# Performance work log

Hardware: AMD Instinct MI355X
Metric: run time of the kernel (lower is better)

## Reference

```python
import jax, jax.numpy as jnp
import numpy as np

N = 50000      # nodes (single node type 'tx')
E = 400000     # edges per edge type ('fwd' and 'rev')
F_IN = 128     # input feature dim
F = 128        # cfg.gnn.dim_inner
H = 8          # attention heads
D = F // H     # per-head dim
L = 2          # cfg.gnn.layers_mp
C = 2          # dim_out (fraud logits)


def setup_inputs() -> dict:
    key = jax.random.key(0)
    k = jax.random.split(key, 12)
    f32 = jnp.float32
    g = lambda kk, sh, fan: jax.random.normal(kk, sh, f32) / np.float32(np.sqrt(fan))
    return dict(
        x=jax.random.normal(k[0], (N, F_IN), f32),
        edge_index_fwd=jax.random.randint(k[1], (2, E), 0, N),
        edge_index_rev=jax.random.randint(k[2], (2, E), 0, N),
        in_w=g(k[3], (F_IN, F), F_IN),
        in_b=jnp.zeros((F,), f32),
        kqv_w=g(k[4], (L, F, 3 * F), F),
        kqv_b=jnp.zeros((L, 3 * F), f32),
        krel_w=g(k[5], (L, 2, H, D, D), D),
        vrel_w=g(k[6], (L, 2, H, D, D), D),
        p_rel=jnp.ones((L, 2, H), f32),
        out_w=g(k[7], (L, F, F), F),
        out_b=jnp.zeros((L, F), f32),
        skip=jnp.ones((L,), f32),
        head_w=g(k[8], (F, C), F),
        head_b=jnp.zeros((C,), f32),
    )


def reference(x, edge_index_fwd, edge_index_rev, in_w, in_b, kqv_w, kqv_b,
              krel_w, vrel_w, p_rel, out_w, out_b, skip, head_w, head_b):
    n = x.shape[0]
    ef, er = edge_index_fwd, edge_index_rev
    Ef, Er = ef.shape[1], er.shape[1]
    dst = jnp.concatenate([ef[1], er[1]])                 # [E_tot]
    scale = 1.0 / jnp.sqrt(jnp.asarray(D, x.dtype))

    h = x @ in_w + in_b                                   # in_proj['tx'], [N,F]
    for l in range(L):
        kqv = h @ kqv_w[l] + kqv_b[l]                     # [N,3F]
        k, q, v = jnp.split(kqv, 3, axis=1)
        k = k.reshape(n, H, D)
        q = q.reshape(n, H, D)
        v = v.reshape(n, H, D)
        # per-edge-type relation transforms (head-wise DxD, no bias)
        k_rel = jnp.einsum('nhd,ehdf->enhf', k, krel_w[l])  # [2,N,H,D]
        v_rel = jnp.einsum('nhd,ehdf->enhf', v, vrel_w[l])
        # gather src features per edge type, concatenate edge types
        k_j = jnp.concatenate([k_rel[0][ef[0]], k_rel[1][er[0]]], axis=0)  # [E_tot,H,D]
        v_j = jnp.concatenate([v_rel[0][ef[0]], v_rel[1][er[0]]], axis=0)
        p_e = jnp.concatenate([jnp.broadcast_to(p_rel[l, 0], (Ef, H)),
                               jnp.broadcast_to(p_rel[l, 1], (Er, H))], axis=0)
        q_i = q[dst]                                       # [E_tot,H,D]
        alpha = jnp.einsum('ehd,ehd->eh', q_i, k_j) * p_e * scale
        # segment softmax over all incoming edges of each dst node
        m = jax.ops.segment_max(alpha, dst, num_segments=n)
        ex = jnp.exp(alpha - m[dst])
        denom = jax.ops.segment_sum(ex, dst, num_segments=n)
        w = ex / (denom[dst] + 1e-16)                      # [E_tot,H]
        agg = jax.ops.segment_sum(w[:, :, None] * v_j, dst,
                                  num_segments=n).reshape(n, F)
        a = jax.nn.gelu(agg, approximate=False) @ out_w[l] + out_b[l]
        g = jax.nn.sigmoid(skip[l])
        h = jax.nn.relu(g * a + (1.0 - g) * h)             # skip + act(dropout=0)
    return h @ head_w + head_b                             # logits [N,C]
```

## Files before the change

kernel.cpp:

```cpp
#include <hip/hip_runtime.h>
#include <math.h>

typedef short short8 __attribute__((ext_vector_type(8)));
typedef float f32x4 __attribute__((ext_vector_type(4)));

__device__ __forceinline__ unsigned short f2bf(float f){
    unsigned u = __float_as_uint(f);
    unsigned r = u + 0x7fffu + ((u >> 16) & 1u);
    return (unsigned short)(r >> 16);
}

__global__ void k_count(const int* __restrict__ ef, const int* __restrict__ er,
                        int* __restrict__ deg, int Ef, int Er)
{
    int Etot = Ef + Er;
    for (int e = blockIdx.x*blockDim.x + threadIdx.x; e < Etot; e += gridDim.x*blockDim.x) {
        int dst = (e < Ef) ? ef[Ef + e] : er[Er + (e - Ef)];
        atomicAdd(&deg[dst], 1);
    }
}

__global__ void k_chunk_sums(const int* __restrict__ deg, int* __restrict__ csum, int n)
{
    __shared__ int s[256];
    int t = threadIdx.x, i = blockIdx.x*256 + t;
    s[t] = (i < n) ? deg[i] : 0;
    __syncthreads();
    for (int off = 128; off > 0; off >>= 1) {
        if (t < off) s[t] += s[t + off];
        __syncthreads();
    }
    if (t == 0) csum[blockIdx.x] = s[0];
}

__global__ void k_scan_chunks(int* __restrict__ csum, int nch)
{
    __shared__ int s[1024];
    int t = threadIdx.x;
    int v = (t < nch) ? csum[t] : 0;
    s[t] = v; __syncthreads();
    for (int off = 1; off < 1024; off <<= 1) {
        int u = (t >= off) ? s[t - off] : 0;
        __syncthreads();
        s[t] += u;
        __syncthreads();
    }
    if (t < nch) csum[t] = s[t] - v;
}

__global__ void k_rowstart(const int* __restrict__ deg, const int* __restrict__ csum,
                           int* __restrict__ row_start, int* __restrict__ cursor, int n)
{
    __shared__ int s[256];
    int t = threadIdx.x, i = blockIdx.x*256 + t;
    int d = (i < n) ? deg[i] : 0;
    s[t] = d; __syncthreads();
    for (int off = 1; off < 256; off <<= 1) {
        int u = (t >= off) ? s[t - off] : 0;
        __syncthreads();
        s[t] += u;
        __syncthreads();
    }
    if (i <= n) {
        int rs = csum[blockIdx.x] + s[t] - d;
        row_start[i] = rs;
        cursor[i] = rs;
    }
}

__global__ void k_fill(const int* __restrict__ ef, const int* __restrict__ er,
                       int* __restrict__ cursor, unsigned* __restrict__ srcs,
                       int Ef, int Er, int n_nodes)
{
    int Etot = Ef + Er;
    if (blockIdx.x == 0 && threadIdx.x == 0) { srcs[Etot] = 0; srcs[Etot + 1] = 0; }
    for (int e = blockIdx.x*blockDim.x + threadIdx.x; e < Etot; e += gridDim.x*blockDim.x) {
        int src, dst, tt;
        if (e < Ef) { src = ef[e]; dst = ef[Ef + e]; tt = 0; }
        else { int e2 = e - Ef; src = er[e2]; dst = er[Er + e2]; tt = 1; }
        int pos = atomicAdd(&cursor[dst], 1);
        srcs[pos] = (unsigned)(tt*n_nodes + src)*32u;
    }
}

__global__ void k_setup(const float* __restrict__ kqv_w, const float* __restrict__ kqv_b,
                        const float* __restrict__ krel_w, const float* __restrict__ vrel_w,
                        const float* __restrict__ p_rel, const float* __restrict__ out_w,
                        const float* __restrict__ out_b, const float* __restrict__ in_w,
                        const float* __restrict__ x, const float* __restrict__ head_b,
                        unsigned short* __restrict__ WcT, float* __restrict__ biasc,
                        unsigned short* __restrict__ WoT, float* __restrict__ biaso,
                        unsigned short* __restrict__ WiT, unsigned short* __restrict__ x16,
                        int* __restrict__ deg, float* __restrict__ logits, int n_nodes)
{
    const int N0 = 2*129*640;
    const int N1 = N0 + 2*129*128;
    const int N2 = N1 + 128*128;
    const long long N3 = (long long)N2 + (long long)n_nodes*32;
    const long long N4 = N3 + n_nodes;
    const long long N5 = N4 + 2*n_nodes;

    for (long long idx = (long long)blockIdx.x*blockDim.x + threadIdx.x; idx < N5;
         idx += (long long)gridDim.x*blockDim.x) {
        if (idx < N0) {
            int i = (int)idx;
            int l = i / (129*640);
            int rem = i % (129*640);
            int r = rem / 640, c = rem % 640;
            float val;
            if (c < 128) {
                val = (r < 128) ? kqv_w[((size_t)l*128 + r)*384 + 128 + c]
                                : kqv_b[l*384 + 128 + c];
            } else {
                int c2 = c - 128;
                int tt = c2 >> 8;
                int cc = c2 & 255;
                int f = cc >> 1;
                int part = cc & 1;
                int hh = f >> 4, fd = f & 15;
                const float* rw = (part == 0 ? krel_w : vrel_w)
                                  + (((size_t)(l*2 + tt)*8 + hh)*16)*16 + fd;
                int base_col = (part == 0 ? 0 : 256) + hh*16;
                float s = 0.f;
                #pragma unroll
                for (int d = 0; d < 16; ++d) {
                    float a = (r < 128) ? kqv_w[((size_t)l*128 + r)*384 + base_col + d]
                                        : kqv_b[l*384 + base_col + d];
                    s += a * rw[d*16];
                }
                if (part == 0) s *= p_rel[(l*2 + tt)*8 + hh] * 0.25f * 1.4426950408889634f;
                val = s;
            }
            if (r < 128) WcT[((size_t)l*640 + c)*128 + r] = f2bf(val);
            else         biasc[l*640 + c] = val;
        } else if (idx < N1) {
            int i = (int)(idx - N0);
            int l = i / (129*128);
            int rem = i % (129*128);
            int r = rem / 128, c = rem % 128;
            if (r < 128) WoT[((size_t)l*128 + c)*128 + r] = f2bf(out_w[((size_t)l*128 + r)*128 + c]);
            else         biaso[l*128 + c] = out_b[l*128 + c];
        } else if (idx < N2) {
            int i = (int)(idx - N1);
            int r = i >> 7, c = i & 127;
            WiT[(size_t)c*128 + r] = f2bf(in_w[(size_t)r*128 + c]);
        } else if (idx < N3) {
            long long i = idx - N2;
            float4 v = *(const float4*)&x[i*4];
            uint2 w;
            w.x = (unsigned)f2bf(v.x) | ((unsigned)f2bf(v.y) << 16);
            w.y = (unsigned)f2bf(v.z) | ((unsigned)f2bf(v.w) << 16);
            *(uint2*)&x16[i*4] = w;
        } else if (idx < N4) {
            deg[idx - N3] = 0;
        } else {
            long long i = idx - N4;
            logits[i] = head_b[i & 1];
        }
    }
}

__global__ __launch_bounds__(256) void k_mfma(
    const unsigned short* __restrict__ A16, const unsigned short* __restrict__ WT,
    const float* __restrict__ biasc, float* __restrict__ out_f,
    unsigned short* __restrict__ out_b16, unsigned* __restrict__ kv,
    const float* __restrict__ skip, const float* __restrict__ hw,
    float* __restrict__ logits, int l,
    int n_nodes, int R, int C, int mode)
{
    __shared__ uint4 As[64*16];
    __shared__ uint4 Ws[64*16];
    int b = blockIdx.x;
    int xcd = b & 7, jj = b >> 3;
    int r_t = (jj / C)*8 + xcd;
    int c_t = jj % C;
    if (r_t >= R) return;
    int n0 = r_t*64, c0 = c_t*64;
    int t = threadIdx.x;

    #pragma unroll
    for (int it = 0; it < 4; ++it) {
        int gi = t + it*256;
        int m = gi >> 4, g = gi & 15;
        uint4 a = *(const uint4*)&A16[((size_t)(n0 + m)*16 + g)*8];
        As[m*16 + (g ^ (m & 15))] = a;
    }
    #pragma unroll
    for (int it = 0; it < 4; ++it) {
        int gi = t + it*256;
        int cw = gi >> 4, g = gi & 15;
        uint4 wv = *(const uint4*)&WT[((size_t)(c0 + cw)*16 + g)*8];
        Ws[cw*16 + (g ^ (cw & 15))] = wv;
    }
    __syncthreads();

    int lane = t & 63, w = t >> 6;
    int lm = lane & 15, quad = lane >> 4;
    f32x4 acc[4];
    #pragma unroll
    for (int i = 0; i < 4; ++i) { acc[i][0]=0.f; acc[i][1]=0.f; acc[i][2]=0.f; acc[i][3]=0.f; }

    #pragma unroll
    for (int chunk = 0; chunk < 4; ++chunk) {
        int gq = chunk*4 + quad;
        short8 bfrag = *(const short8*)&Ws[(w*16 + lm)*16 + (gq ^ lm)];
        #pragma unroll
        for (int i = 0; i < 4; ++i) {
            short8 afrag = *(const short8*)&As[(i*16 + lm)*16 + (gq ^ lm)];
            acc[i] = __builtin_amdgcn_mfma_f32_16x16x32_bf16(afrag, bfrag, acc[i], 0, 0, 0);
        }
    }

    int c = c0 + w*16 + lm;
    float bc = biasc[c];
    if (mode == 3) {
        float g = 1.f/(1.f + expf(-skip[l]));
        float hw0 = hw[c*2], hw1 = hw[c*2 + 1];
        #pragma unroll
        for (int i = 0; i < 4; ++i) {
            #pragma unroll
            for (int rr = 0; rr < 4; ++rr) {
                int m = n0 + i*16 + quad*4 + rr;
                float nv = 0.f;
                if (m < n_nodes) {
                    float hv = out_f[(size_t)m*128 + c];
                    nv = fmaxf(g*(acc[i][rr] + bc) + (1.f - g)*hv, 0.f);
                }
                float p0 = nv*hw0, p1 = nv*hw1;
                p0 += __shfl_xor(p0, 1); p1 += __shfl_xor(p1, 1);
                p0 += __shfl_xor(p0, 2); p1 += __shfl_xor(p1, 2);
                p0 += __shfl_xor(p0, 4); p1 += __shfl_xor(p1, 4);
                p0 += __shfl_xor(p0, 8); p1 += __shfl_xor(p1, 8);
                if (lm == 0 && m < n_nodes) {
                    atomicAdd(&logits[m*2],     p0);
                    atomicAdd(&logits[m*2 + 1], p1);
                }
            }
        }
    } else if (mode == 2) {
        float g = 1.f/(1.f + expf(-skip[l]));
        #pragma unroll
        for (int i = 0; i < 4; ++i) {
            #pragma unroll
            for (int rr = 0; rr < 4; ++rr) {
                int m = n0 + i*16 + quad*4 + rr;
                if (m < n_nodes) {
                    size_t o = (size_t)m*128 + c;
                    float hv = out_f[o];
                    float nv = fmaxf(g*(acc[i][rr] + bc) + (1.f - g)*hv, 0.f);
                    out_f[o] = nv;
                    out_b16[o] = f2bf(nv);
                }
            }
        }
    } else if (mode == 0) {
        #pragma unroll
        for (int i = 0; i < 4; ++i) {
            #pragma unroll
            for (int rr = 0; rr < 4; ++rr) {
                int m = n0 + i*16 + quad*4 + rr;
                if (m < n_nodes) {
                    size_t o = (size_t)m*128 + c;
                    float nv = acc[i][rr] + bc;
                    out_f[o] = nv;
                    out_b16[o] = f2bf(nv);
                }
            }
        }
    } else if (c0 < 128) {
        #pragma unroll
        for (int i = 0; i < 4; ++i) {
            #pragma unroll
            for (int rr = 0; rr < 4; ++rr) {
                int m = n0 + i*16 + quad*4 + rr;
                if (m < n_nodes) out_f[(size_t)m*128 + c] = acc[i][rr] + bc;
            }
        }
    } else {
        int c2 = c - 128;
        int tt = c2 >> 8;
        int f = (c2 & 255) >> 1;
        unsigned* dst = kv + (size_t)tt*n_nodes*128;
        bool isk = (lane & 1) == 0;
        #pragma unroll
        for (int i = 0; i < 4; ++i) {
            #pragma unroll
            for (int rr = 0; rr < 4; ++rr) {
                float val = acc[i][rr] + bc;
                float other = __shfl_xor(val, 1);
                int m = n0 + i*16 + quad*4 + rr;
                if (isk && m < n_nodes) {
                    unsigned wd = ((unsigned)f2bf(val) << 16) | (unsigned)f2bf(other);
                    dst[(size_t)m*128 + f] = wd;
                }
            }
        }
    }
}

__global__ __launch_bounds__(256) void k_attn(
    const unsigned* __restrict__ srcs, const int* __restrict__ row_start,
    const uint4* __restrict__ kv, const float* __restrict__ qa,
    unsigned short* __restrict__ qa16, int n_nodes)
{
    int lane = threadIdx.x & 31;
    int n = blockIdx.x*8 + (threadIdx.x >> 5);
    if (n >= n_nodes) return;
    float4 q4 = *(const float4*)&qa[(size_t)n*128 + lane*4];
    int s = row_start[n], e = row_start[n + 1];

    float m0 = -INFINITY, l0 = 0.f; float4 a0 = make_float4(0.f,0.f,0.f,0.f);
    float m1 = -INFINITY, l1 = 0.f; float4 a1 = make_float4(0.f,0.f,0.f,0.f);

    uint4 w0n = kv[srcs[s] + lane];
    uint4 w1n = kv[srcs[s + 1] + lane];
    int pos = s;
    for (; pos + 1 < e; pos += 2) {
        uint4 w0 = w0n, w1 = w1n;
        unsigned sv0 = srcs[pos + 2], sv1 = srcs[pos + 3];
        w0n = kv[sv0 + lane];
        w1n = kv[sv1 + lane];
        float d0 = __uint_as_float(w0.x & 0xffff0000u)*q4.x
                 + __uint_as_float(w0.y & 0xffff0000u)*q4.y
                 + __uint_as_float(w0.z & 0xffff0000u)*q4.z
                 + __uint_as_float(w0.w & 0xffff0000u)*q4.w;
        float d1 = __uint_as_float(w1.x & 0xffff0000u)*q4.x
                 + __uint_as_float(w1.y & 0xffff0000u)*q4.y
                 + __uint_as_float(w1.z & 0xffff0000u)*q4.z
                 + __uint_as_float(w1.w & 0xffff0000u)*q4.w;
        d0 += __shfl_xor(d0, 1); d1 += __shfl_xor(d1, 1);
        d0 += __shfl_xor(d0, 2); d1 += __shfl_xor(d1, 2);
        float mn0 = fmaxf(m0, d0), mn1 = fmaxf(m1, d1);
        float sc0 = exp2f(m0 - mn0), sc1 = exp2f(m1 - mn1);
        float wt0 = exp2f(d0 - mn0), wt1 = exp2f(d1 - mn1);
        l0 = l0*sc0 + wt0;               l1 = l1*sc1 + wt1;
        a0.x = a0.x*sc0 + wt0*__uint_as_float(w0.x << 16);
        a1.x = a1.x*sc1 + wt1*__uint_as_float(w1.x << 16);
        a0.y = a0.y*sc0 + wt0*__uint_as_float(w0.y << 16);
        a1.y = a1.y*sc1 + wt1*__uint_as_float(w1.y << 16);
        a0.z = a0.z*sc0 + wt0*__uint_as_float(w0.z << 16);
        a1.z = a1.z*sc1 + wt1*__uint_as_float(w1.z << 16);
        a0.w = a0.w*sc0 + wt0*__uint_as_float(w0.w << 16);
        a1.w = a1.w*sc1 + wt1*__uint_as_float(w1.w << 16);
        m0 = mn0; m1 = mn1;
    }
    if (pos < e) {
        uint4 w0 = w0n;
        float d = __uint_as_float(w0.x & 0xffff0000u)*q4.x
                + __uint_as_float(w0.y & 0xffff0000u)*q4.y
                + __uint_as_float(w0.z & 0xffff0000u)*q4.z
                + __uint_as_float(w0.w & 0xffff0000u)*q4.w;
        d += __shfl_xor(d, 1);
        d += __shfl_xor(d, 2);
        float mn = fmaxf(m0, d);
        float sc = exp2f(m0 - mn);
        float wt = exp2f(d - mn);
        l0 = l0*sc + wt;
        a0.x = a0.x*sc + wt*__uint_as_float(w0.x << 16);
        a0.y = a0.y*sc + wt*__uint_as_float(w0.y << 16);
        a0.z = a0.z*sc + wt*__uint_as_float(w0.z << 16);
        a0.w = a0.w*sc + wt*__uint_as_float(w0.w << 16);
        m0 = mn;
    }
    float mn = fmaxf(m0, m1);
    float sc0 = (m0 == -INFINITY) ? 0.f : exp2f(m0 - mn);
    float sc1 = (m1 == -INFINITY) ? 0.f : exp2f(m1 - mn);
    float lsum = l0*sc0 + l1*sc1;
    float4 acc;
    acc.x = a0.x*sc0 + a1.x*sc1;
    acc.y = a0.y*sc0 + a1.y*sc1;
    acc.z = a0.z*sc0 + a1.z*sc1;
    acc.w = a0.w*sc0 + a1.w*sc1;

    float inv = 1.f/(lsum + 1e-16f);
    float x0 = acc.x*inv, x1 = acc.y*inv, x2 = acc.z*inv, x3 = acc.w*inv;
    float g0 = 0.5f*x0*(1.f + erff(x0*0.70710678118654752f));
    float g1 = 0.5f*x1*(1.f + erff(x1*0.70710678118654752f));
    float g2 = 0.5f*x2*(1.f + erff(x2*0.70710678118654752f));
    float g3 = 0.5f*x3*(1.f + erff(x3*0.70710678118654752f));
    uint2 pk;
    pk.x = (unsigned)f2bf(g0) | ((unsigned)f2bf(g1) << 16);
    pk.y = (unsigned)f2bf(g2) | ((unsigned)f2bf(g3) << 16);
    *(uint2*)&qa16[(size_t)n*128 + lane*4] = pk;
}

extern "C" void kernel_launch(void* const* d_in, const int* in_sizes, int n_in,
                              void* d_out, int out_size, void* d_ws, size_t ws_size,
                              hipStream_t stream)
{
    const float* x      = (const float*)d_in[0];
    const int*   ef     = (const int*)d_in[1];
    const int*   er     = (const int*)d_in[2];
    const float* in_w   = (const float*)d_in[3];
    const float* in_b   = (const float*)d_in[4];
    const float* kqv_w  = (const float*)d_in[5];
    const float* kqv_b  = (const float*)d_in[6];
    const float* krel_w = (const float*)d_in[7];
    const float* vrel_w = (const float*)d_in[8];
    const float* p_rel  = (const float*)d_in[9];
    const float* out_w  = (const float*)d_in[10];
    const float* out_b  = (const float*)d_in[11];
    const float* skip   = (const float*)d_in[12];
    const float* head_w = (const float*)d_in[13];
    const float* head_b = (const float*)d_in[14];
    float* out = (float*)d_out;

    int n_nodes = in_sizes[0] / 128;
    int Ef = in_sizes[1] / 2, Er = in_sizes[2] / 2;
    int Etot = Ef + Er;
    int nch = (n_nodes + 255)/256;
    int ntile = (n_nodes + 63)/64;
    int npad = ntile*64;

    float* p = (float*)d_ws;
    float* h    = p; p += (size_t)npad*128;
    float* qa   = p; p += (size_t)npad*128;
    unsigned* kv = (unsigned*)p; p += (size_t)2*n_nodes*128;
    unsigned short* h16  = (unsigned short*)p; p += (size_t)npad*128/2;
    unsigned short* qa16 = (unsigned short*)p; p += (size_t)npad*128/2;
    unsigned short* x16  = (unsigned short*)p; p += (size_t)npad*128/2;
    unsigned short* WiT = (unsigned short*)p; p += (size_t)(128*128)/2;
    unsigned short* WcT = (unsigned short*)p; p += (size_t)(2*640*128)/2;
    float* biasc = p; p += 2*640;
    unsigned short* WoT = (unsigned short*)p; p += (size_t)(2*128*128)/2;
    float* biaso = p; p += 2*128;
    int* deg       = (int*)p;      p += n_nodes;
    int* csum      = (int*)p;      p += 1024;
    int* row_start = (int*)p;      p += n_nodes + 1;
    int* cursor    = (int*)p;      p += n_nodes + 1;
    unsigned* srcs = (unsigned*)p; p += Etot + 2;

    int Rg = (ntile + 7)/8;

    k_setup<<<7500, 256, 0, stream>>>(kqv_w, kqv_b, krel_w, vrel_w, p_rel, out_w, out_b,
                                      in_w, x, head_b, WcT, biasc, WoT, biaso, WiT, x16,
                                      deg, out, n_nodes);
    k_count<<<1024, 256, 0, stream>>>(ef, er, deg, Ef, Er);
    k_chunk_sums<<<nch, 256, 0, stream>>>(deg, csum, n_nodes);
    k_scan_chunks<<<1, 1024, 0, stream>>>(csum, nch);
    k_rowstart<<<(n_nodes + 256)/256, 256, 0, stream>>>(deg, csum, row_start, cursor, n_nodes);
    k_fill<<<1024, 256, 0, stream>>>(ef, er, cursor, srcs, Ef, Er, n_nodes);

    k_mfma<<<Rg*8*2, 256, 0, stream>>>(x16, WiT, in_b, h, h16, kv, skip, head_w, out, 0,
                                       n_nodes, ntile, 2, 0);
    for (int l = 0; l < 2; ++l) {
        k_mfma<<<Rg*8*10, 256, 0, stream>>>(h16, WcT + (size_t)l*640*128,
                                            biasc + l*640, qa, nullptr, kv, skip,
                                            head_w, out, l, n_nodes, ntile, 10, 1);
        k_attn<<<(n_nodes + 7)/8, 256, 0, stream>>>(srcs, row_start,
                                                    (const uint4*)kv, qa, qa16, n_nodes);
        int omode = (l == 1) ? 3 : 2;
        k_mfma<<<Rg*8*2, 256, 0, stream>>>(qa16, WoT + (size_t)l*128*128,
                                           biaso + l*128, h, h16, kv, skip,
                                           head_w, out, l, n_nodes, ntile, 2, omode);
    }
}
```

Measured before the change: 444.9 us.

## Drop fp32 copies of h and q; keep them only in bf16 with packed stores

Removes the fp32 hidden-state and query buffers. The residual h and the attention query q are now stored and read only as bf16, and the epilogues write pairs of bf16 values as packed 32-bit words through a lane shuffle. This cuts global memory traffic in the GEMM epilogues and the attention query load. In exchange, the skip-connection residual and the query lose precision across layers. The mode 2 epilogue also reads h16 and writes it back in place, which is safe only because each tile owns its own rows and columns.

```diff
diff --git a/kernel.cpp b/kernel.cpp
--- a/kernel.cpp
+++ b/kernel.cpp
@@ -8,6 +8,9 @@
     unsigned u = __float_as_uint(f);
     unsigned r = u + 0x7fffu + ((u >> 16) & 1u);
     return (unsigned short)(r >> 16);
+}
+__device__ __forceinline__ float bf2f(unsigned short s){
+    return __uint_as_float((unsigned)s << 16);
 }
 
 __global__ void k_count(const int* __restrict__ ef, const int* __restrict__ er,
@@ -162,8 +165,8 @@
 
 __global__ __launch_bounds__(256) void k_mfma(
     const unsigned short* __restrict__ A16, const unsigned short* __restrict__ WT,
-    const float* __restrict__ biasc, float* __restrict__ out_f,
-    unsigned short* __restrict__ out_b16, unsigned* __restrict__ kv,
+    const float* __restrict__ biasc, unsigned short* __restrict__ q16,
+    unsigned short* __restrict__ h16, unsigned* __restrict__ kv,
     const float* __restrict__ skip, const float* __restrict__ hw,
     float* __restrict__ logits, int l,
     int n_nodes, int R, int C, int mode)
@@ -213,6 +216,7 @@
 
     int c = c0 + w*16 + lm;
     float bc = biasc[c];
+    bool even = (lane & 1) == 0;
     if (mode == 3) {
         float g = 1.f/(1.f + expf(-skip[l]));
         float hw0 = hw[c*2], hw1 = hw[c*2 + 1];
@@ -223,7 +227,7 @@
                 int m = n0 + i*16 + quad*4 + rr;
                 float nv = 0.f;
                 if (m < n_nodes) {
-                    float hv = out_f[(size_t)m*128 + c];
+                    float hv = bf2f(h16[(size_t)m*128 + c]);
                     nv = fmaxf(g*(acc[i][rr] + bc) + (1.f - g)*hv, 0.f);
                 }
                 float p0 = nv*hw0, p1 = nv*hw1;
@@ -239,41 +243,46 @@
         }
     } else if (mode == 2) {
         float g = 1.f/(1.f + expf(-skip[l]));
+        unsigned* dst = (unsigned*)h16;
         #pragma unroll
         for (int i = 0; i < 4; ++i) {
             #pragma unroll
             for (int rr = 0; rr < 4; ++rr) {
                 int m = n0 + i*16 + quad*4 + rr;
-                if (m < n_nodes) {
-                    size_t o = (size_t)m*128 + c;
-                    float hv = out_f[o];
-                    float nv = fmaxf(g*(acc[i][rr] + bc) + (1.f - g)*hv, 0.f);
-                    out_f[o] = nv;
-                    out_b16[o] = f2bf(nv);
-                }
+                float hv = (m < n_nodes) ? bf2f(h16[(size_t)m*128 + c]) : 0.f;
+                float nv = fmaxf(g*(acc[i][rr] + bc) + (1.f - g)*hv, 0.f);
+                float other = __shfl_xor(nv, 1);
+                if (even && m < n_nodes)
+                    dst[(size_t)m*64 + (c >> 1)] =
+                        (unsigned)f2bf(nv) | ((unsigned)f2bf(other) << 16);
             }
         }
     } else if (mode == 0) {
+        unsigned* dst = (unsigned*)h16;
         #pragma unroll
         for (int i = 0; i < 4; ++i) {
             #pragma unroll
             for (int rr = 0; rr < 4; ++rr) {
                 int m = n0 + i*16 + quad*4 + rr;
-                if (m < n_nodes) {
-                    size_t o = (size_t)m*128 + c;
-                    float nv = acc[i][rr] + bc;
-                    out_f[o] = nv;
-                    out_b16[o] = f2bf(nv);
-                }
+                float nv = acc[i][rr] + bc;
+                float other = __shfl_xor(nv, 1);
+                if (even && m < n_nodes)
+                    dst[(size_t)m*64 + (c >> 1)] =
+                        (unsigned)f2bf(nv) | ((unsigned)f2bf(other) << 16);
             }
         }
     } else if (c0 < 128) {
+        unsigned* dst = (unsigned*)q16;
         #pragma unroll
         for (int i = 0; i < 4; ++i) {
             #pragma unroll
             for (int rr = 0; rr < 4; ++rr) {
+                float val = acc[i][rr] + bc;
+                float other = __shfl_xor(val, 1);
                 int m = n0 + i*16 + quad*4 + rr;
-                if (m < n_nodes) out_f[(size_t)m*128 + c] = acc[i][rr] + bc;
+                if (even && m < n_nodes)
+                    dst[(size_t)m*64 + (c >> 1)] =
+                        (unsigned)f2bf(val) | ((unsigned)f2bf(other) << 16);
             }
         }
     } else {
@@ -281,7 +290,6 @@
         int tt = c2 >> 8;
         int f = (c2 & 255) >> 1;
         unsigned* dst = kv + (size_t)tt*n_nodes*128;
-        bool isk = (lane & 1) == 0;
         #pragma unroll
         for (int i = 0; i < 4; ++i) {
             #pragma unroll
@@ -289,7 +297,7 @@
                 float val = acc[i][rr] + bc;
                 float other = __shfl_xor(val, 1);
                 int m = n0 + i*16 + quad*4 + rr;
-                if (isk && m < n_nodes) {
+                if (even && m < n_nodes) {
                     unsigned wd = ((unsigned)f2bf(val) << 16) | (unsigned)f2bf(other);
                     dst[(size_t)m*128 + f] = wd;
                 }
@@ -300,13 +308,18 @@
 
 __global__ __launch_bounds__(256) void k_attn(
     const unsigned* __restrict__ srcs, const int* __restrict__ row_start,
-    const uint4* __restrict__ kv, const float* __restrict__ qa,
+    const uint4* __restrict__ kv, const unsigned short* __restrict__ q16,
     unsigned short* __restrict__ qa16, int n_nodes)
 {
     int lane = threadIdx.x & 31;
     int n = blockIdx.x*8 + (threadIdx.x >> 5);
     if (n >= n_nodes) return;
-    float4 q4 = *(const float4*)&qa[(size_t)n*128 + lane*4];
+    uint2 qp = *(const uint2*)&q16[(size_t)n*128 + lane*4];
+    float4 q4;
+    q4.x = __uint_as_float(qp.x << 16);
+    q4.y = __uint_as_float(qp.x & 0xffff0000u);
+    q4.z = __uint_as_float(qp.y << 16);
+    q4.w = __uint_as_float(qp.y & 0xffff0000u);
     int s = row_start[n], e = row_start[n + 1];
 
     float m0 = -INFINITY, l0 = 0.f; float4 a0 = make_float4(0.f,0.f,0.f,0.f);
@@ -413,10 +426,9 @@
     int npad = ntile*64;
 
     float* p = (float*)d_ws;
-    float* h    = p; p += (size_t)npad*128;
-    float* qa   = p; p += (size_t)npad*128;
     unsigned* kv = (unsigned*)p; p += (size_t)2*n_nodes*128;
     unsigned short* h16  = (unsigned short*)p; p += (size_t)npad*128/2;
+    unsigned short* q16  = (unsigned short*)p; p += (size_t)npad*128/2;
     unsigned short* qa16 = (unsigned short*)p; p += (size_t)npad*128/2;
     unsigned short* x16  = (unsigned short*)p; p += (size_t)npad*128/2;
     unsigned short* WiT = (unsigned short*)p; p += (size_t)(128*128)/2;
@@ -441,17 +453,17 @@
     k_rowstart<<<(n_nodes + 256)/256, 256, 0, stream>>>(deg, csum, row_start, cursor, n_nodes);
     k_fill<<<1024, 256, 0, stream>>>(ef, er, cursor, srcs, Ef, Er, n_nodes);
 
-    k_mfma<<<Rg*8*2, 256, 0, stream>>>(x16, WiT, in_b, h, h16, kv, skip, head_w, out, 0,
-                                       n_nodes, ntile, 2, 0);
+    k_mfma<<<Rg*8*2, 256, 0, stream>>>(x16, WiT, in_b, nullptr, h16, kv, skip,
+                                       head_w, out, 0, n_nodes, ntile, 2, 0);
     for (int l = 0; l < 2; ++l) {
         k_mfma<<<Rg*8*10, 256, 0, stream>>>(h16, WcT + (size_t)l*640*128,
-                                            biasc + l*640, qa, nullptr, kv, skip,
+                                            biasc + l*640, q16, nullptr, kv, skip,
                                             head_w, out, l, n_nodes, ntile, 10, 1);
         k_attn<<<(n_nodes + 7)/8, 256, 0, stream>>>(srcs, row_start,
-                                                    (const uint4*)kv, qa, qa16, n_nodes);
+                                                    (const uint4*)kv, q16, qa16, n_nodes);
         int omode = (l == 1) ? 3 : 2;
         k_mfma<<<Rg*8*2, 256, 0, stream>>>(qa16, WoT + (size_t)l*128*128,
-                                           biaso + l*128, h, h16, kv, skip,
+                                           biaso + l*128, nullptr, h16, kv, skip,
                                            head_w, out, l, n_nodes, ntile, 2, omode);
     }
 }
```

New measurement: 441.9 us. Within noise of the previous version (-0.7%).
